# Kernel tuning notes

Measured on AMD Instinct MI355X. Metric: run time of the kernel, lower is better.

Reference implementation:

```python
import jax, jax.numpy as jnp
from jax import lax
import numpy as np

N_DFT = 1024
N_HOP = 256
N_FILTER = N_DFT // 2 + 1  # 513
AMIN = 1e-10
DYNAMIC_RANGE = 80.0


def _make_dft_kernels(n_dft):
    """Real/imag DFT kernels with periodic Hann window, shape (n_dft, 1, n_filter) for WIO conv."""
    nb = n_dft // 2 + 1
    t = np.arange(n_dft)
    w = np.arange(nb) * 2.0 * np.pi / float(n_dft)
    real = np.cos(w[:, None] * t[None, :])           # (nb, n_dft)
    imag = -np.sin(w[:, None] * t[None, :])
    # scipy periodic ('fftbins=True') hann window
    win = 0.5 - 0.5 * np.cos(2.0 * np.pi * t / float(n_dft))
    real = (real * win).T[:, None, :]                # (n_dft, 1, nb) = (W, I, O)
    imag = (imag * win).T[:, None, :]
    return real.astype(np.float32), imag.astype(np.float32)


def setup_inputs() -> dict:
    key = jax.random.key(0)
    x = jax.random.normal(key, (32, 2, 262144), dtype=jnp.float32)  # (batch, n_ch, len_src)
    kr, ki = _make_dft_kernels(N_DFT)
    return {"x": x, "k_real": jnp.asarray(kr), "k_imag": jnp.asarray(ki)}


def reference(x, k_real, k_imag):
    B, CH, L = x.shape
    xm = x.reshape(B * CH, L, 1)  # treat each audio channel as an independent mono signal
    dn = ("NWC", "WIO", "NWC")
    conv = lambda k: lax.conv_general_dilated(
        xm, k, window_strides=(N_HOP,), padding="SAME", dimension_numbers=dn
    )
    # power spectrogram: real^2 + imag^2 -> (B*CH, n_frame, n_filter)
    power = conv(k_real) ** 2 + conv(k_imag) ** 2
    n_frame = power.shape[1]
    # -> (B, n_filter, n_frame, CH)  (channels_last image format)
    spec = power.reshape(B, CH, n_frame, N_FILTER).transpose(0, 3, 2, 1)
    # power_spectrogram == 2.0, so no pow; return_decibel_spectrogram == True:
    log_spec = 10.0 * jnp.log10(jnp.maximum(spec, AMIN))
    log_spec = log_spec - jnp.max(log_spec, axis=(1, 2, 3), keepdims=True)
    return jnp.maximum(log_spec, -DYNAMIC_RANGE)
```

## Files before the change

kernel.cpp:

```cpp
#include <hip/hip_runtime.h>
#include <math.h>

namespace {
constexpr int NDFT   = 1024;
constexpr int NHOP   = 256;
constexpr int NFILT  = 513;
constexpr int LSRC   = 262144;
constexpr int NFRAME = 1024;
constexpr int PAD_L  = 384;
constexpr long PER_B = (long)NFILT * NFRAME * 2;

constexpr int KT2 = 16;
constexpr int CHUNK_US = 8192;
constexpr size_t WSB2_BYTES = (size_t)8 * KT2 * CHUNK_US * 2;
constexpr size_t PLANE_ELEMS_PER_SIG = 1024 * 512;

constexpr int KT1 = 32;
constexpr size_t WS_B_BYTES = (size_t)8 * KT1 * CHUNK_US * 2;
}

using short8 = __attribute__((ext_vector_type(8))) short;
using f32x4  = __attribute__((ext_vector_type(4))) float;

__device__ __forceinline__ unsigned int f2key(float f) {
    unsigned int u = __float_as_uint(f);
    return (u & 0x80000000u) ? ~u : (u | 0x80000000u);
}
__device__ __forceinline__ float key2f(unsigned int k) {
    return (k & 0x80000000u) ? __uint_as_float(k ^ 0x80000000u) : __uint_as_float(~k);
}
__device__ __forceinline__ unsigned short bf16rn(float v) {
    unsigned int u = __float_as_uint(v);
    return (unsigned short)((u + 0x7fffu + ((u >> 16) & 1u)) >> 16);
}

__global__ void zero_ws(unsigned int* __restrict__ w) {
    if (threadIdx.x < 32) w[threadIdx.x] = 0u;
}

__global__ __launch_bounds__(256) void fold_split(
    const float* __restrict__ x,
    unsigned short* __restrict__ sH, unsigned short* __restrict__ sL,
    unsigned short* __restrict__ dH, unsigned short* __restrict__ dL,
    int sig0)
{
    const int floc = blockIdx.x * 4 + (threadIdx.x >> 6);
    const int grp  = threadIdx.x & 63;
    const int sig  = sig0 + (floc >> 10);
    const int fl   = floc & 1023;
    const long sbase = (long)sig * LSRC;
    const int st   = fl * NHOP - PAD_L;
    const int s0   = grp * 8;

    const float xmid = x[sbase + st + 512];

    float fw[8], bw[8];
    if (fl >= 2 && fl <= 1021) {
        const float4 a0 = *reinterpret_cast<const float4*>(x + sbase + st + s0);
        const float4 a1 = *reinterpret_cast<const float4*>(x + sbase + st + s0 + 4);
        fw[0]=a0.x; fw[1]=a0.y; fw[2]=a0.z; fw[3]=a0.w;
        fw[4]=a1.x; fw[5]=a1.y; fw[6]=a1.z; fw[7]=a1.w;
        const long q0 = sbase + st + 1017 - s0;
        const float4 b0 = *reinterpret_cast<const float4*>(x + q0 - 1);
        const float4 b1 = *reinterpret_cast<const float4*>(x + q0 + 3);
        const float  b2 = x[q0 + 7];
        const float va[8] = {b0.y, b0.z, b0.w, b1.x, b1.y, b1.z, b1.w, b2};
        #pragma unroll
        for (int j = 0; j < 8; ++j) bw[j] = va[7 - j];
    } else {
        #pragma unroll
        for (int j = 0; j < 8; ++j) {
            const int s = s0 + j;
            const int p1 = st + s;
            const int p2 = st + 1024 - s;
            fw[j] = ((unsigned)p1 < (unsigned)LSRC) ? x[sbase + p1] : 0.0f;
            bw[j] = ((unsigned)p2 < (unsigned)LSRC) ? x[sbase + p2] : 0.0f;
        }
    }

    union { unsigned short u[8]; uint4 v; } shv, slv, dhv, dlv;
    #pragma unroll
    for (int j = 0; j < 8; ++j) {
        float x1 = fw[j], x2 = bw[j];
        if (j == 0 && s0 == 0) { x1 = xmid; x2 = 0.0f; }
        const float sm = x1 + x2;
        const float df = x1 - x2;
        const unsigned short h1 = bf16rn(sm);
        shv.u[j] = h1;
        slv.u[j] = bf16rn(sm - __uint_as_float((unsigned int)h1 << 16));
        const unsigned short h2 = bf16rn(df);
        dhv.u[j] = h2;
        dlv.u[j] = bf16rn(df - __uint_as_float((unsigned int)h2 << 16));
    }
    const size_t wo = (size_t)floc * 512 + s0;
    *reinterpret_cast<uint4*>(sH + wo) = shv.v;
    *reinterpret_cast<uint4*>(sL + wo) = slv.v;
    *reinterpret_cast<uint4*>(dH + wo) = dhv.v;
    *reinterpret_cast<uint4*>(dL + wo) = dlv.v;
}

__global__ __launch_bounds__(256) void build_B2(const float* __restrict__ kr,
                                                const float* __restrict__ ki,
                                                unsigned short* __restrict__ wsB)
{
    const int nt = blockIdx.x >> 4;
    const int kt = blockIdx.x & 15;
    unsigned short* chunk = wsB + (size_t)blockIdx.x * CHUNK_US;
    const int col = threadIdx.x >> 1;
    const int h   = threadIdx.x & 1;
    const int bin = nt * 64 + (col & 63);
    const float* src = (col < 64) ? kr : ki;
    #pragma unroll
    for (int j = 0; j < 4; ++j) {
        const int sl = h * 4 + j;
        const int c  = sl & 3;
        union { unsigned short u[8]; uint4 v; } pk;
        #pragma unroll
        for (int i = 0; i < 8; ++i) {
            const int s = kt * 32 + c * 8 + i;
            const int t = (s == 0) ? 512 : s;
            const float v = src[t * NFILT + bin];
            const unsigned short hi = bf16rn(v);
            pk.u[i] = h ? bf16rn(v - __uint_as_float((unsigned int)hi << 16)) : hi;
        }
        *reinterpret_cast<uint4*>(&chunk[col * 64 + ((sl ^ (col & 7)) << 3)]) = pk.v;
    }
}

__global__ __launch_bounds__(256, 2) void spec_gemm2(
    const unsigned short* __restrict__ sH, const unsigned short* __restrict__ sL,
    const unsigned short* __restrict__ dH, const unsigned short* __restrict__ dL,
    const unsigned short* __restrict__ wsB,
    float* __restrict__ out, unsigned int* __restrict__ wmax,
    int sig0, int nsig)
{
    __shared__ unsigned short smem[2 * 128 * 64];

    const int tid  = threadIdx.x;
    const int lane = tid & 63, w = tid >> 6;
    const int wm = w >> 1, wn = w & 1;
    const int l15 = lane & 15, l16 = lane >> 4;

    const int phys = blockIdx.x;
    const int xcd  = phys & 7, slot = phys >> 3;
    const int nt   = slot & 7;
    const int mt   = xcd * nsig + (slot >> 3);
    const int sig  = sig0 + (mt >> 3);
    const int f0   = (mt & 7) * 128;
    const unsigned short* bchunks = wsB + (size_t)nt * KT2 * CHUNK_US;

    const unsigned short* __restrict__ pH = wn ? dH : sH;
    const unsigned short* __restrict__ pL = wn ? dL : sL;

    size_t aoff[4];
    #pragma unroll
    for (int mf = 0; mf < 4; ++mf) {
        const int row = wm * 64 + mf * 16 + l15;
        aoff[mf] = (size_t)(mt * 128 + row) * 512 + l16 * 8;
    }

    f32x4 acc[4][4];
    #pragma unroll
    for (int i = 0; i < 4; ++i)
        #pragma unroll
        for (int j = 0; j < 4; ++j)
            #pragma unroll
            for (int r = 0; r < 4; ++r) acc[i][j][r] = 0.0f;

    #define LOAD_B(ktv, nb)                                                    \
        {                                                                      \
            const char* g = (const char*)(bchunks + (size_t)(ktv) * CHUNK_US); \
            char* l = (char*)smem + (nb) * 16384;                              \
            _Pragma("unroll")                                                  \
            for (int i = 0; i < 4; ++i) {                                      \
                const int off = i * 4096 + w * 1024;                           \
                __builtin_amdgcn_global_load_lds(                              \
                    (const __attribute__((address_space(1))) unsigned int*)(g + off + lane * 16), \
                    (__attribute__((address_space(3))) unsigned int*)(l + off), \
                    16, 0, 0);                                                 \
            }                                                                  \
        }

    #define LOAD_A(ktv, AH, AL)                                                \
        {                                                                      \
            _Pragma("unroll")                                                  \
            for (int mf = 0; mf < 4; ++mf) {                                   \
                const size_t o = aoff[mf] + (size_t)(ktv) * 32;                \
                AH[mf] = *reinterpret_cast<const short8*>(pH + o);             \
                AL[mf] = *reinterpret_cast<const short8*>(pL + o);             \
            }                                                                  \
        }

    #define MFMA_STEP(AH, AL, nb)                                              \
        {                                                                      \
            __builtin_amdgcn_s_setprio(1);                                     \
            _Pragma("unroll")                                                  \
            for (int nf = 0; nf < 4; ++nf) {                                   \
                const int col = wn * 64 + nf * 16 + l15;                       \
                const unsigned short* bb = smem + (nb) * 8192 + col * 64;      \
                const short8 bh = *reinterpret_cast<const short8*>(bb + ((l16 ^ (col & 7)) << 3));       \
                const short8 bl = *reinterpret_cast<const short8*>(bb + (((4 + l16) ^ (col & 7)) << 3)); \
                _Pragma("unroll")                                              \
                for (int mf = 0; mf < 4; ++mf) {                               \
                    acc[mf][nf] = __builtin_amdgcn_mfma_f32_16x16x32_bf16(AH[mf], bh, acc[mf][nf], 0, 0, 0); \
                    acc[mf][nf] = __builtin_amdgcn_mfma_f32_16x16x32_bf16(AL[mf], bh, acc[mf][nf], 0, 0, 0); \
                    acc[mf][nf] = __builtin_amdgcn_mfma_f32_16x16x32_bf16(AH[mf], bl, acc[mf][nf], 0, 0, 0); \
                }                                                              \
            }                                                                  \
            __builtin_amdgcn_s_setprio(0);                                     \
        }

    short8 ah0[4], al0[4], ah1[4], al1[4];

    LOAD_A(0, ah0, al0)
    LOAD_B(0, 0)
    __syncthreads();

    #pragma unroll 1
    for (int kt = 0; kt < KT2; kt += 2) {
        LOAD_A(kt + 1, ah1, al1)
        LOAD_B(kt + 1, 1)
        MFMA_STEP(ah0, al0, 0)
        __syncthreads();
        if (kt + 2 < KT2) {
            LOAD_A(kt + 2, ah0, al0)
            LOAD_B(kt + 2, 0)
        }
        MFMA_STEP(ah1, al1, 1)
        __syncthreads();
    }
    #undef LOAD_A
    #undef LOAD_B
    #undef MFMA_STEP

    if (wn == 0) {
        #pragma unroll
        for (int mf = 0; mf < 4; ++mf)
            #pragma unroll
            for (int nf = 0; nf < 4; ++nf) {
                const int binl = nf * 16 + l15;
                #pragma unroll
                for (int r = 0; r < 4; ++r) {
                    const int row = wm * 64 + mf * 16 + l16 * 4 + r;
                    const float v = acc[mf][nf][r];
                    smem[row * 68 + binl] = bf16rn(v * v);
                }
            }
    }
    __syncthreads();
    if (wn == 1) {
        const int batch = sig >> 1, ch = sig & 1;
        float lmax = -3.0e38f;
        #pragma unroll
        for (int mf = 0; mf < 4; ++mf)
            #pragma unroll
            for (int nf = 0; nf < 4; ++nf) {
                const int binl = nf * 16 + l15;
                const int bin  = nt * 64 + binl;
                #pragma unroll
                for (int r = 0; r < 4; ++r) {
                    const int row = wm * 64 + mf * 16 + l16 * 4 + r;
                    const float v = acc[mf][nf][r];
                    const float re2 = __uint_as_float((unsigned int)smem[row * 68 + binl] << 16);
                    const float p = re2 + v * v;
                    const float d = 10.0f * log10f(fmaxf(p, 1e-10f));
                    const int frame = f0 + row;
                    out[((long)(batch * NFILT + bin) * NFRAME + frame) * 2 + ch] = d;
                    lmax = fmaxf(lmax, d);
                }
            }
        #pragma unroll
        for (int off = 32; off > 0; off >>= 1) lmax = fmaxf(lmax, __shfl_xor(lmax, off));
        if (lane == 0) atomicMax(&wmax[batch], f2key(lmax));
    }
}

__global__ __launch_bounds__(256) void build_B(const float* __restrict__ kr,
                                               const float* __restrict__ ki,
                                               unsigned short* __restrict__ wsB)
{
    const int nt = blockIdx.x >> 5;
    const int kt = blockIdx.x & 31;
    unsigned short* chunk = wsB + (size_t)blockIdx.x * CHUNK_US;
    const int col = threadIdx.x >> 1;
    const int h   = threadIdx.x & 1;
    const int bin = nt * 64 + (col >> 1);
    const float* src = (col & 1) ? ki : kr;
    #pragma unroll
    for (int j = 0; j < 4; ++j) {
        const int sl = h * 4 + j;
        const int c  = sl & 3;
        union { unsigned short u[8]; uint4 v; } pk;
        #pragma unroll
        for (int i = 0; i < 8; ++i) {
            const int t = kt * 32 + c * 8 + i;
            const float v = src[t * NFILT + bin];
            const unsigned short hi = bf16rn(v);
            pk.u[i] = h ? bf16rn(v - __uint_as_float((unsigned int)hi << 16)) : hi;
        }
        *reinterpret_cast<uint4*>(&chunk[col * 64 + ((sl ^ (col & 7)) << 3)]) = pk.v;
    }
}

__global__ __launch_bounds__(256, 2) void spec_gemm_mid(
    const float* __restrict__ x, const unsigned short* __restrict__ wsB,
    float* __restrict__ out, unsigned int* __restrict__ wmax)
{
    __shared__ unsigned short Ad[2][128][64];
    __shared__ unsigned short Bd[2][128][64];

    const int tid  = threadIdx.x;
    const int lane = tid & 63, w = tid >> 6;
    const int wm = w >> 1, wn = w & 1;
    const int l15 = lane & 15, l16 = lane >> 4;
    const int mt = blockIdx.x, nt = blockIdx.y;
    const int sig = mt >> 3, f0 = (mt & 7) * 128;
    const long sb = (long)sig * LSRC;

    const int arow = tid >> 1, ac2 = tid & 1;
    const int abase_p = (f0 + arow) * NHOP - PAD_L + ac2 * 16;
    const unsigned short* bchunks = wsB + (size_t)nt * KT1 * CHUNK_US;

    f32x4 acc[4][4];
    #pragma unroll
    for (int i = 0; i < 4; ++i)
        #pragma unroll
        for (int j = 0; j < 4; ++j)
            #pragma unroll
            for (int r = 0; r < 4; ++r) acc[i][j][r] = 0.0f;

    float va[16];

    #define LOAD_A(ktv)                                                        \
        {                                                                      \
            const int p0 = abase_p + (ktv) * 32;                               \
            if (p0 >= 0 && p0 + 16 <= LSRC) {                                  \
                *reinterpret_cast<float4*>(&va[0])  = *reinterpret_cast<const float4*>(x + sb + p0);      \
                *reinterpret_cast<float4*>(&va[4])  = *reinterpret_cast<const float4*>(x + sb + p0 + 4);  \
                *reinterpret_cast<float4*>(&va[8])  = *reinterpret_cast<const float4*>(x + sb + p0 + 8);  \
                *reinterpret_cast<float4*>(&va[12]) = *reinterpret_cast<const float4*>(x + sb + p0 + 12); \
            } else {                                                           \
                _Pragma("unroll")                                              \
                for (int i = 0; i < 16; ++i) {                                 \
                    const int p = p0 + i;                                      \
                    va[i] = (p >= 0 && p < LSRC) ? x[sb + p] : 0.0f;           \
                }                                                              \
            }                                                                  \
        }

    #define LOAD_B(ktv, nb)                                                    \
        {                                                                      \
            const char* g = (const char*)(bchunks + (size_t)(ktv) * CHUNK_US); \
            char* l = (char*)&Bd[nb][0][0];                                    \
            _Pragma("unroll")                                                  \
            for (int i = 0; i < 4; ++i) {                                      \
                const int off = i * 4096 + w * 1024;                           \
                __builtin_amdgcn_global_load_lds(                              \
                    (const __attribute__((address_space(1))) unsigned int*)(g + off + lane * 16), \
                    (__attribute__((address_space(3))) unsigned int*)(l + off), \
                    16, 0, 0);                                                 \
            }                                                                  \
        }

    #define WRITE_A(nb)                                                       \
        {                                                                      \
            unsigned short* ab = &Ad[nb][arow][0];                             \
            _Pragma("unroll")                                                  \
            for (int j = 0; j < 2; ++j) {                                      \
                union { unsigned short u[8]; uint4 v; } hv, lv;                \
                _Pragma("unroll")                                              \
                for (int i = 0; i < 8; ++i) {                                  \
                    const float vv = va[j * 8 + i];                            \
                    const unsigned short hi = bf16rn(vv);                      \
                    hv.u[i] = hi;                                              \
                    lv.u[i] = bf16rn(vv - __uint_as_float((unsigned int)hi << 16)); \
                }                                                              \
                const int c = ac2 * 2 + j;                                     \
                *reinterpret_cast<uint4*>(ab + (((c) ^ (arow & 7)) << 3))     = hv.v; \
                *reinterpret_cast<uint4*>(ab + (((4 + c) ^ (arow & 7)) << 3)) = lv.v; \
            }                                                                  \
        }

    LOAD_A(0)
    LOAD_B(0, 0)
    WRITE_A(0)
    __syncthreads();

    #pragma unroll 1
    for (int kt = 0; kt < KT1; ++kt) {
        const int cur = kt & 1, nxt = cur ^ 1;
        const bool pf = (kt + 1 < KT1);
        if (pf) {
            LOAD_A(kt + 1)
            LOAD_B(kt + 1, nxt)
        }
        short8 ah[4], al[4];
        #pragma unroll
        for (int mf = 0; mf < 4; ++mf) {
            const int row = wm * 64 + mf * 16 + l15;
            const unsigned short* ab = &Ad[cur][row][0];
            ah[mf] = *reinterpret_cast<const short8*>(ab + ((l16 ^ (row & 7)) << 3));
            al[mf] = *reinterpret_cast<const short8*>(ab + (((4 + l16) ^ (row & 7)) << 3));
        }
        __builtin_amdgcn_s_setprio(1);
        #pragma unroll
        for (int nf = 0; nf < 4; ++nf) {
            const int col = wn * 64 + nf * 16 + l15;
            const unsigned short* bb = &Bd[cur][col][0];
            const short8 bh = *reinterpret_cast<const short8*>(bb + ((l16 ^ (col & 7)) << 3));
            const short8 bl = *reinterpret_cast<const short8*>(bb + (((4 + l16) ^ (col & 7)) << 3));
            #pragma unroll
            for (int mf = 0; mf < 4; ++mf) {
                acc[mf][nf] = __builtin_amdgcn_mfma_f32_16x16x32_bf16(ah[mf], bh, acc[mf][nf], 0, 0, 0);
                acc[mf][nf] = __builtin_amdgcn_mfma_f32_16x16x32_bf16(al[mf], bh, acc[mf][nf], 0, 0, 0);
                acc[mf][nf] = __builtin_amdgcn_mfma_f32_16x16x32_bf16(ah[mf], bl, acc[mf][nf], 0, 0, 0);
            }
        }
        __builtin_amdgcn_s_setprio(0);
        if (pf) WRITE_A(nxt)
        __syncthreads();
    }
    #undef LOAD_A
    #undef LOAD_B
    #undef WRITE_A

    const int batch = sig >> 1, ch = sig & 1;
    float lmax = -3.0e38f;
    #pragma unroll
    for (int mf = 0; mf < 4; ++mf)
        #pragma unroll
        for (int nf = 0; nf < 4; ++nf) {
            const int col = nt * 128 + wn * 64 + nf * 16 + l15;
            const int bin = col >> 1;
            #pragma unroll
            for (int r = 0; r < 4; ++r) {
                const float v  = acc[mf][nf][r];
                const float sq = v * v;
                const float p  = sq + __shfl_xor(sq, 1);
                if (!(lane & 1)) {
                    const int frame = f0 + wm * 64 + mf * 16 + l16 * 4 + r;
                    const float d = 10.0f * log10f(fmaxf(p, 1e-10f));
                    out[((long)(batch * NFILT + bin) * NFRAME + frame) * 2 + ch] = d;
                    lmax = fmaxf(lmax, d);
                }
            }
        }
    #pragma unroll
    for (int off = 32; off > 0; off >>= 1) lmax = fmaxf(lmax, __shfl_xor(lmax, off));
    if (lane == 0) atomicMax(&wmax[batch], f2key(lmax));
}

__global__ __launch_bounds__(256, 2) void spec_nyq(
    const float* __restrict__ x, const float* __restrict__ kr,
    const float* __restrict__ ki, float* __restrict__ out,
    unsigned int* __restrict__ wmax)
{
    __shared__ float xs[17152];
    __shared__ float kc[1024], ks[1024];
    const int sig = blockIdx.x >> 4, ft = blockIdx.x & 15;
    const int f0 = ft * 64;
    const long sb = (long)sig * LSRC;
    const int start = f0 * NHOP - PAD_L;
    for (int i = threadIdx.x; i < 17152; i += 256) {
        const int p = start + i;
        xs[i] = (p >= 0 && p < LSRC) ? x[sb + p] : 0.0f;
    }
    for (int t = threadIdx.x; t < 1024; t += 256) {
        kc[t] = kr[t * NFILT + 512];
        ks[t] = ki[t * NFILT + 512];
    }
    __syncthreads();
    const int fr = threadIdx.x >> 2, q = threadIdx.x & 3;
    const int rot = ((fr + q) & 7) * 4;
    float re = 0.0f, im = 0.0f;
    #pragma unroll 4
    for (int j = 0; j < 256; j += 4) {
        const int je = (j + rot) & 255;
        const float4 a = *reinterpret_cast<const float4*>(&xs[fr * 256 + q * 256 + je]);
        const float4 c = *reinterpret_cast<const float4*>(&kc[q * 256 + je]);
        const float4 s = *reinterpret_cast<const float4*>(&ks[q * 256 + je]);
        re = fmaf(a.x, c.x, re); re = fmaf(a.y, c.y, re);
        re = fmaf(a.z, c.z, re); re = fmaf(a.w, c.w, re);
        im = fmaf(a.x, s.x, im); im = fmaf(a.y, s.y, im);
        im = fmaf(a.z, s.z, im); im = fmaf(a.w, s.w, im);
    }
    re += __shfl_xor(re, 1); re += __shfl_xor(re, 2);
    im += __shfl_xor(im, 1); im += __shfl_xor(im, 2);
    const int batch = sig >> 1, ch = sig & 1;
    float lmax = -3.0e38f;
    if (q == 0) {
        const float p = re * re + im * im;
        const float d = 10.0f * log10f(fmaxf(p, 1e-10f));
        out[((long)(batch * NFILT + 512) * NFRAME + (f0 + fr)) * 2 + ch] = d;
        lmax = d;
    }
    #pragma unroll
    for (int off = 32; off > 0; off >>= 1) lmax = fmaxf(lmax, __shfl_xor(lmax, off));
    if ((threadIdx.x & 63) == 0) atomicMax(&wmax[batch], f2key(lmax));
}

__global__ __launch_bounds__(256) void finalize(
    float* __restrict__ out, const unsigned int* __restrict__ wmax, long n4)
{
    const long stride = (long)gridDim.x * 256;
    for (long i4 = blockIdx.x * 256L + threadIdx.x; i4 < n4; i4 += stride) {
        const long i = i4 * 4;
        const int b  = (int)(i / PER_B);
        const float m = key2f(wmax[b]);
        float4 v = reinterpret_cast<float4*>(out)[i4];
        v.x = fmaxf(v.x - m, -80.0f);
        v.y = fmaxf(v.y - m, -80.0f);
        v.z = fmaxf(v.z - m, -80.0f);
        v.w = fmaxf(v.w - m, -80.0f);
        reinterpret_cast<float4*>(out)[i4] = v;
    }
}

namespace fb {
constexpr int TILE_F = 32;
constexpr int SPAN   = (TILE_F - 1) * NHOP + NDFT;
}

__global__ __launch_bounds__(256) void spec_main_fb(
    const float* __restrict__ x, const float* __restrict__ kr,
    const float* __restrict__ ki, float* __restrict__ out,
    unsigned int* __restrict__ wmax)
{
    __shared__ float xs[fb::SPAN];
    const int s   = blockIdx.x;
    const int f0  = blockIdx.y * fb::TILE_F;
    const int tid = threadIdx.x;
    const long sig_base = (long)s * LSRC;
    const int start = f0 * NHOP - PAD_L;
    for (int i = tid; i < fb::SPAN; i += 256) {
        const int p = start + i;
        xs[i] = (p >= 0 && p < LSRC) ? x[sig_base + p] : 0.0f;
    }
    __syncthreads();
    const int b0 = tid, b1 = tid + 256;
    float ar0[fb::TILE_F], ai0[fb::TILE_F], ar1[fb::TILE_F], ai1[fb::TILE_F];
    #pragma unroll
    for (int f = 0; f < fb::TILE_F; ++f) { ar0[f]=0.f; ai0[f]=0.f; ar1[f]=0.f; ai1[f]=0.f; }
    #pragma unroll 1
    for (int t = 0; t < NDFT; t += 4) {
        float br0[4], bq0[4], br1[4], bq1[4];
        #pragma unroll
        for (int j = 0; j < 4; ++j) {
            br0[j] = kr[(t + j) * NFILT + b0]; bq0[j] = ki[(t + j) * NFILT + b0];
            br1[j] = kr[(t + j) * NFILT + b1]; bq1[j] = ki[(t + j) * NFILT + b1];
        }
        #pragma unroll
        for (int f = 0; f < fb::TILE_F; ++f) {
            const float4 a = *reinterpret_cast<const float4*>(&xs[t + NHOP * f]);
            ar0[f]=fmaf(a.x,br0[0],ar0[f]); ar0[f]=fmaf(a.y,br0[1],ar0[f]);
            ar0[f]=fmaf(a.z,br0[2],ar0[f]); ar0[f]=fmaf(a.w,br0[3],ar0[f]);
            ai0[f]=fmaf(a.x,bq0[0],ai0[f]); ai0[f]=fmaf(a.y,bq0[1],ai0[f]);
            ai0[f]=fmaf(a.z,bq0[2],ai0[f]); ai0[f]=fmaf(a.w,bq0[3],ai0[f]);
            ar1[f]=fmaf(a.x,br1[0],ar1[f]); ar1[f]=fmaf(a.y,br1[1],ar1[f]);
            ar1[f]=fmaf(a.z,br1[2],ar1[f]); ar1[f]=fmaf(a.w,br1[3],ar1[f]);
            ai1[f]=fmaf(a.x,bq1[0],ai1[f]); ai1[f]=fmaf(a.y,bq1[1],ai1[f]);
            ai1[f]=fmaf(a.z,bq1[2],ai1[f]); ai1[f]=fmaf(a.w,bq1[3],ai1[f]);
        }
    }
    const int b = s >> 1, ch = s & 1;
    float lmax = -3.0e38f;
    #pragma unroll
    for (int f = 0; f < fb::TILE_F; ++f) {
        const int frame = f0 + f;
        const float p0 = ar0[f]*ar0[f] + ai0[f]*ai0[f];
        const float p1 = ar1[f]*ar1[f] + ai1[f]*ai1[f];
        const float d0 = 10.0f * log10f(fmaxf(p0, 1e-10f));
        const float d1 = 10.0f * log10f(fmaxf(p1, 1e-10f));
        lmax = fmaxf(lmax, fmaxf(d0, d1));
        out[((long)(b * NFILT + b0) * NFRAME + frame) * 2 + ch] = d0;
        out[((long)(b * NFILT + b1) * NFRAME + frame) * 2 + ch] = d1;
    }
    #pragma unroll
    for (int off = 32; off > 0; off >>= 1) lmax = fmaxf(lmax, __shfl_xor(lmax, off));
    if ((tid & 63) == 0) atomicMax(&wmax[b], f2key(lmax));
}

__global__ __launch_bounds__(256) void spec_nyq_fb(
    const float* __restrict__ x, const float* __restrict__ kr,
    const float* __restrict__ ki, float* __restrict__ out,
    unsigned int* __restrict__ wmax)
{
    const int gid   = blockIdx.x * 256 + threadIdx.x;
    const int s     = gid >> 10;
    const int frame = gid & 1023;
    const float* xp = x + (long)s * LSRC;
    const int start = frame * NHOP - PAD_L;
    float re = 0.f, im = 0.f;
    for (int t = 0; t < NDFT; ++t) {
        const int idx = start + t;
        const float a = (idx >= 0 && idx < LSRC) ? xp[idx] : 0.0f;
        re = fmaf(a, kr[t * NFILT + 512], re);
        im = fmaf(a, ki[t * NFILT + 512], im);
    }
    const float p = re * re + im * im;
    const float d = 10.0f * log10f(fmaxf(p, 1e-10f));
    const int b = s >> 1, ch = s & 1;
    out[((long)(b * NFILT + 512) * NFRAME + frame) * 2 + ch] = d;
    float lmax = d;
    #pragma unroll
    for (int off = 32; off > 0; off >>= 1) lmax = fmaxf(lmax, __shfl_xor(lmax, off));
    if ((threadIdx.x & 63) == 0) atomicMax(&wmax[b], f2key(lmax));
}

extern "C" void kernel_launch(void* const* d_in, const int* in_sizes, int n_in,
                              void* d_out, int out_size, void* d_ws, size_t ws_size,
                              hipStream_t stream) {
    const float* x  = (const float*)d_in[0];
    const float* kr = (const float*)d_in[1];
    const float* ki = (const float*)d_in[2];
    float* out = (float*)d_out;
    const long n4 = (long)out_size / 4;

    int nsig = 0;
    const int cands[4] = {64, 32, 16, 8};
    for (int c = 0; c < 4; ++c) {
        const size_t need = 128 + WSB2_BYTES + (size_t)cands[c] * 4 * 1048576;
        if (ws_size >= need) { nsig = cands[c]; break; }
    }

    if (nsig) {
        unsigned int* wmax   = (unsigned int*)d_ws;
        unsigned short* wsB2 = (unsigned short*)((char*)d_ws + 128);
        unsigned short* sH   = (unsigned short*)((char*)d_ws + 128 + WSB2_BYTES);
        const size_t pe = (size_t)nsig * PLANE_ELEMS_PER_SIG;
        unsigned short* sL = sH + pe;
        unsigned short* dH = sL + pe;
        unsigned short* dL = dH + pe;
        zero_ws<<<1, 64, 0, stream>>>(wmax);
        build_B2<<<128, 256, 0, stream>>>(kr, ki, wsB2);
        const int npass = 64 / nsig;
        for (int p = 0; p < npass; ++p) {
            fold_split<<<nsig * 256, 256, 0, stream>>>(x, sH, sL, dH, dL, p * nsig);
            spec_gemm2<<<nsig * 64, 256, 0, stream>>>(sH, sL, dH, dL, wsB2, out, wmax,
                                                      p * nsig, nsig);
        }
        spec_nyq<<<1024, 256, 0, stream>>>(x, kr, ki, out, wmax);
        finalize<<<2048, 256, 0, stream>>>(out, wmax, n4);
    } else if (ws_size >= WS_B_BYTES + 128) {
        unsigned short* wsB = (unsigned short*)d_ws;
        unsigned int* wmax  = (unsigned int*)((char*)d_ws + WS_B_BYTES);
        zero_ws<<<1, 64, 0, stream>>>(wmax);
        build_B<<<8 * KT1, 256, 0, stream>>>(kr, ki, wsB);
        spec_gemm_mid<<<dim3(512, 8), 256, 0, stream>>>(x, wsB, out, wmax);
        spec_nyq<<<1024, 256, 0, stream>>>(x, kr, ki, out, wmax);
        finalize<<<2048, 256, 0, stream>>>(out, wmax, n4);
    } else {
        unsigned int* wmax = (unsigned int*)d_ws;
        zero_ws<<<1, 64, 0, stream>>>(wmax);
        dim3 grid(64, NFRAME / fb::TILE_F);
        spec_main_fb<<<grid, 256, 0, stream>>>(x, kr, ki, out, wmax);
        spec_nyq_fb<<<(64 * NFRAME) / 256, 256, 0, stream>>>(x, kr, ki, out, wmax);
        finalize<<<2048, 256, 0, stream>>>(out, wmax, n4);
    }
}
```

Before: 622.7 us.

## Split spec_gemm2 across 8 waves with narrower per-wave tiles and single A buffer

Doubles the block to 512 threads (8 waves), so each wave computes a 64x32 output tile instead of 64x64. A-fragment register double buffering is removed: A for the next k-step is now loaded after the current MFMA step, which cuts register use and allows more resident waves (launch bounds 512,4). The B LDS load is split across more waves. The cost is less latency hiding for A loads, since each load is issued just before the barrier, and more redundant A loads per block because wave pairs share rows.

```diff
diff --git a/kernel.cpp b/kernel.cpp
--- a/kernel.cpp
+++ b/kernel.cpp
@@ -127,7 +127,7 @@
     }
 }
 
-__global__ __launch_bounds__(256, 2) void spec_gemm2(
+__global__ __launch_bounds__(512, 4) void spec_gemm2(
     const unsigned short* __restrict__ sH, const unsigned short* __restrict__ sL,
     const unsigned short* __restrict__ dH, const unsigned short* __restrict__ dL,
     const unsigned short* __restrict__ wsB,
@@ -138,7 +138,7 @@
 
     const int tid  = threadIdx.x;
     const int lane = tid & 63, w = tid >> 6;
-    const int wm = w >> 1, wn = w & 1;
+    const int wm = w >> 2, wn = w & 3;
     const int l15 = lane & 15, l16 = lane >> 4;
 
     const int phys = blockIdx.x;
@@ -149,21 +149,16 @@
     const int f0   = (mt & 7) * 128;
     const unsigned short* bchunks = wsB + (size_t)nt * KT2 * CHUNK_US;
 
-    const unsigned short* __restrict__ pH = wn ? dH : sH;
-    const unsigned short* __restrict__ pL = wn ? dL : sL;
-
-    size_t aoff[4];
-    #pragma unroll
-    for (int mf = 0; mf < 4; ++mf) {
-        const int row = wm * 64 + mf * 16 + l15;
-        aoff[mf] = (size_t)(mt * 128 + row) * 512 + l16 * 8;
-    }
-
-    f32x4 acc[4][4];
+    const unsigned short* __restrict__ pH = (wn >= 2) ? dH : sH;
+    const unsigned short* __restrict__ pL = (wn >= 2) ? dL : sL;
+
+    const size_t abase = (size_t)(mt * 128 + wm * 64 + l15) * 512 + l16 * 8;
+
+    f32x4 acc[4][2];
     #pragma unroll
     for (int i = 0; i < 4; ++i)
         #pragma unroll
-        for (int j = 0; j < 4; ++j)
+        for (int j = 0; j < 2; ++j)
             #pragma unroll
             for (int r = 0; r < 4; ++r) acc[i][j][r] = 0.0f;
 
@@ -172,8 +167,8 @@
             const char* g = (const char*)(bchunks + (size_t)(ktv) * CHUNK_US); \
             char* l = (char*)smem + (nb) * 16384;                              \
             _Pragma("unroll")                                                  \
-            for (int i = 0; i < 4; ++i) {                                      \
-                const int off = i * 4096 + w * 1024;                           \
+            for (int i = 0; i < 2; ++i) {                                      \
+                const int off = i * 8192 + w * 1024;                           \
                 __builtin_amdgcn_global_load_lds(                              \
                     (const __attribute__((address_space(1))) unsigned int*)(g + off + lane * 16), \
                     (__attribute__((address_space(3))) unsigned int*)(l + off), \
@@ -181,64 +176,62 @@
             }                                                                  \
         }
 
-    #define LOAD_A(ktv, AH, AL)                                                \
+    #define LOAD_A(ktv)                                                        \
         {                                                                      \
             _Pragma("unroll")                                                  \
             for (int mf = 0; mf < 4; ++mf) {                                   \
-                const size_t o = aoff[mf] + (size_t)(ktv) * 32;                \
-                AH[mf] = *reinterpret_cast<const short8*>(pH + o);             \
-                AL[mf] = *reinterpret_cast<const short8*>(pL + o);             \
+                const size_t o = abase + (size_t)mf * 8192 + (size_t)(ktv) * 32; \
+                ah[mf] = *reinterpret_cast<const short8*>(pH + o);             \
+                al[mf] = *reinterpret_cast<const short8*>(pL + o);             \
             }                                                                  \
         }
 
-    #define MFMA_STEP(AH, AL, nb)                                              \
+    #define MFMA_STEP(nb)                                                      \
         {                                                                      \
             __builtin_amdgcn_s_setprio(1);                                     \
             _Pragma("unroll")                                                  \
-            for (int nf = 0; nf < 4; ++nf) {                                   \
-                const int col = wn * 64 + nf * 16 + l15;                       \
+            for (int nf = 0; nf < 2; ++nf) {                                   \
+                const int col = wn * 32 + nf * 16 + l15;                       \
                 const unsigned short* bb = smem + (nb) * 8192 + col * 64;      \
                 const short8 bh = *reinterpret_cast<const short8*>(bb + ((l16 ^ (col & 7)) << 3));       \
                 const short8 bl = *reinterpret_cast<const short8*>(bb + (((4 + l16) ^ (col & 7)) << 3)); \
                 _Pragma("unroll")                                              \
                 for (int mf = 0; mf < 4; ++mf) {                               \
-                    acc[mf][nf] = __builtin_amdgcn_mfma_f32_16x16x32_bf16(AH[mf], bh, acc[mf][nf], 0, 0, 0); \
-                    acc[mf][nf] = __builtin_amdgcn_mfma_f32_16x16x32_bf16(AL[mf], bh, acc[mf][nf], 0, 0, 0); \
-                    acc[mf][nf] = __builtin_amdgcn_mfma_f32_16x16x32_bf16(AH[mf], bl, acc[mf][nf], 0, 0, 0); \
+                    acc[mf][nf] = __builtin_amdgcn_mfma_f32_16x16x32_bf16(ah[mf], bh, acc[mf][nf], 0, 0, 0); \
+                    acc[mf][nf] = __builtin_amdgcn_mfma_f32_16x16x32_bf16(al[mf], bh, acc[mf][nf], 0, 0, 0); \
+                    acc[mf][nf] = __builtin_amdgcn_mfma_f32_16x16x32_bf16(ah[mf], bl, acc[mf][nf], 0, 0, 0); \
                 }                                                              \
             }                                                                  \
             __builtin_amdgcn_s_setprio(0);                                     \
         }
 
-    short8 ah0[4], al0[4], ah1[4], al1[4];
-
-    LOAD_A(0, ah0, al0)
+    short8 ah[4], al[4];
+
+    LOAD_A(0)
     LOAD_B(0, 0)
     __syncthreads();
 
     #pragma unroll 1
     for (int kt = 0; kt < KT2; kt += 2) {
-        LOAD_A(kt + 1, ah1, al1)
         LOAD_B(kt + 1, 1)
-        MFMA_STEP(ah0, al0, 0)
+        MFMA_STEP(0)
+        LOAD_A(kt + 1)
         __syncthreads();
-        if (kt + 2 < KT2) {
-            LOAD_A(kt + 2, ah0, al0)
-            LOAD_B(kt + 2, 0)
-        }
-        MFMA_STEP(ah1, al1, 1)
+        if (kt + 2 < KT2) LOAD_B(kt + 2, 0)
+        MFMA_STEP(1)
+        if (kt + 2 < KT2) LOAD_A(kt + 2)
         __syncthreads();
     }
     #undef LOAD_A
     #undef LOAD_B
     #undef MFMA_STEP
 
-    if (wn == 0) {
+    if (wn < 2) {
         #pragma unroll
         for (int mf = 0; mf < 4; ++mf)
             #pragma unroll
-            for (int nf = 0; nf < 4; ++nf) {
-                const int binl = nf * 16 + l15;
+            for (int nf = 0; nf < 2; ++nf) {
+                const int binl = wn * 32 + nf * 16 + l15;
                 #pragma unroll
                 for (int r = 0; r < 4; ++r) {
                     const int row = wm * 64 + mf * 16 + l16 * 4 + r;
@@ -248,14 +241,14 @@
             }
     }
     __syncthreads();
-    if (wn == 1) {
+    if (wn >= 2) {
         const int batch = sig >> 1, ch = sig & 1;
         float lmax = -3.0e38f;
         #pragma unroll
         for (int mf = 0; mf < 4; ++mf)
             #pragma unroll
-            for (int nf = 0; nf < 4; ++nf) {
-                const int binl = nf * 16 + l15;
+            for (int nf = 0; nf < 2; ++nf) {
+                const int binl = (wn - 2) * 32 + nf * 16 + l15;
                 const int bin  = nt * 64 + binl;
                 #pragma unroll
                 for (int r = 0; r < 4; ++r) {
@@ -636,7 +629,7 @@
         const int npass = 64 / nsig;
         for (int p = 0; p < npass; ++p) {
             fold_split<<<nsig * 256, 256, 0, stream>>>(x, sH, sL, dH, dL, p * nsig);
-            spec_gemm2<<<nsig * 64, 256, 0, stream>>>(sH, sL, dH, dL, wsB2, out, wmax,
+            spec_gemm2<<<nsig * 64, 512, 0, stream>>>(sH, sL, dH, dL, wsB2, out, wmax,
                                                       p * nsig, nsig);
         }
         spec_nyq<<<1024, 256, 0, stream>>>(x, kr, ki, out, wmax);
```

Result: slower. 812.2 us (+30.4%).

## Load B fragments directly from global into registers, dropping LDS staging and barriers

Applied to the files above, without the earlier changes.

The GEMM kernel previously staged B chunks into double-buffered shared memory via global_load_lds and synchronized with barriers each k-step. It now loads each wave's B fragments straight from global memory into registers, double-buffered alongside A, and removes the per-step __syncthreads. This cuts LDS traffic, shared memory footprint and barrier stalls, but adds duplicated global/L2 reads of B across waves and more register pressure under launch_bounds(256,2). Shared memory is shrunk to 128x68 for the epilogue use only.

```diff
diff --git a/kernel.cpp b/kernel.cpp
--- a/kernel.cpp
+++ b/kernel.cpp
@@ -134,7 +134,7 @@
     float* __restrict__ out, unsigned int* __restrict__ wmax,
     int sig0, int nsig)
 {
-    __shared__ unsigned short smem[2 * 128 * 64];
+    __shared__ unsigned short smem[128 * 68];
 
     const int tid  = threadIdx.x;
     const int lane = tid & 63, w = tid >> 6;
@@ -158,6 +158,13 @@
         const int row = wm * 64 + mf * 16 + l15;
         aoff[mf] = (size_t)(mt * 128 + row) * 512 + l16 * 8;
     }
+    int boff_h[4], boff_l[4];
+    #pragma unroll
+    for (int nf = 0; nf < 4; ++nf) {
+        const int col = wn * 64 + nf * 16 + l15;
+        boff_h[nf] = col * 64 + ((l16 ^ (col & 7)) << 3);
+        boff_l[nf] = col * 64 + (((4 + l16) ^ (col & 7)) << 3);
+    }
 
     f32x4 acc[4][4];
     #pragma unroll
@@ -166,20 +173,6 @@
         for (int j = 0; j < 4; ++j)
             #pragma unroll
             for (int r = 0; r < 4; ++r) acc[i][j][r] = 0.0f;
-
-    #define LOAD_B(ktv, nb)                                                    \
-        {                                                                      \
-            const char* g = (const char*)(bchunks + (size_t)(ktv) * CHUNK_US); \
-            char* l = (char*)smem + (nb) * 16384;                              \
-            _Pragma("unroll")                                                  \
-            for (int i = 0; i < 4; ++i) {                                      \
-                const int off = i * 4096 + w * 1024;                           \
-                __builtin_amdgcn_global_load_lds(                              \
-                    (const __attribute__((address_space(1))) unsigned int*)(g + off + lane * 16), \
-                    (__attribute__((address_space(3))) unsigned int*)(l + off), \
-                    16, 0, 0);                                                 \
-            }                                                                  \
-        }
 
     #define LOAD_A(ktv, AH, AL)                                                \
         {                                                                      \
@@ -191,43 +184,51 @@
             }                                                                  \
         }
 
-    #define MFMA_STEP(AH, AL, nb)                                              \
+    #define LOAD_B(ktv, BH, BL)                                                \
+        {                                                                      \
+            const unsigned short* c = bchunks + (size_t)(ktv) * CHUNK_US;      \
+            _Pragma("unroll")                                                  \
+            for (int nf = 0; nf < 4; ++nf) {                                   \
+                BH[nf] = *reinterpret_cast<const short8*>(c + boff_h[nf]);     \
+                BL[nf] = *reinterpret_cast<const short8*>(c + boff_l[nf]);     \
+            }                                                                  \
+        }
+
+    #define MFMA_STEP(AH, AL, BH, BL)                                          \
         {                                                                      \
             __builtin_amdgcn_s_setprio(1);                                     \
             _Pragma("unroll")                                                  \
             for (int nf = 0; nf < 4; ++nf) {                                   \
-                const int col = wn * 64 + nf * 16 + l15;                       \
-                const unsigned short* bb = smem + (nb) * 8192 + col * 64;      \
-                const short8 bh = *reinterpret_cast<const short8*>(bb + ((l16 ^ (col & 7)) << 3));       \
-                const short8 bl = *reinterpret_cast<const short8*>(bb + (((4 + l16) ^ (col & 7)) << 3)); \
                 _Pragma("unroll")                                              \
                 for (int mf = 0; mf < 4; ++mf) {                               \
-                    acc[mf][nf] = __builtin_amdgcn_mfma_f32_16x16x32_bf16(AH[mf], bh, acc[mf][nf], 0, 0, 0); \
-                    acc[mf][nf] = __builtin_amdgcn_mfma_f32_16x16x32_bf16(AL[mf], bh, acc[mf][nf], 0, 0, 0); \
-                    acc[mf][nf] = __builtin_amdgcn_mfma_f32_16x16x32_bf16(AH[mf], bl, acc[mf][nf], 0, 0, 0); \
+                    acc[mf][nf] = __builtin_amdgcn_mfma_f32_16x16x32_bf16(AH[mf], BH[nf], acc[mf][nf], 0, 0, 0); \
+                    acc[mf][nf] = __builtin_amdgcn_mfma_f32_16x16x32_bf16(AL[mf], BH[nf], acc[mf][nf], 0, 0, 0); \
+                    acc[mf][nf] = __builtin_amdgcn_mfma_f32_16x16x32_bf16(AH[mf], BL[nf], acc[mf][nf], 0, 0, 0); \
                 }                                                              \
             }                                                                  \
             __builtin_amdgcn_s_setprio(0);                                     \
         }
 
     short8 ah0[4], al0[4], ah1[4], al1[4];
+    short8 bh0[4], bl0[4], bh1[4], bl1[4];
 
     LOAD_A(0, ah0, al0)
-    LOAD_B(0, 0)
-    __syncthreads();
+    LOAD_B(0, bh0, bl0)
+    LOAD_A(1, ah1, al1)
+    LOAD_B(1, bh1, bl1)
 
     #pragma unroll 1
     for (int kt = 0; kt < KT2; kt += 2) {
-        LOAD_A(kt + 1, ah1, al1)
-        LOAD_B(kt + 1, 1)
-        MFMA_STEP(ah0, al0, 0)
-        __syncthreads();
+        MFMA_STEP(ah0, al0, bh0, bl0)
         if (kt + 2 < KT2) {
             LOAD_A(kt + 2, ah0, al0)
-            LOAD_B(kt + 2, 0)
-        }
-        MFMA_STEP(ah1, al1, 1)
-        __syncthreads();
+            LOAD_B(kt + 2, bh0, bl0)
+        }
+        MFMA_STEP(ah1, al1, bh1, bl1)
+        if (kt + 3 < KT2) {
+            LOAD_A(kt + 3, ah1, al1)
+            LOAD_B(kt + 3, bh1, bl1)
+        }
     }
     #undef LOAD_A
     #undef LOAD_B
```

Measured after the change: 626.5 us. No clear change (+0.6%).

## Stage A tiles through LDS via direct global-to-LDS loads in spec_gemm2

Applied to the files above, without the earlier changes.

The A operand (hi/lo bf16 frames) is now loaded from global memory straight into LDS with swizzled global_load_lds, rather than being read into registers per wave. The B tile follows the same path, and the wave layout is remapped so each wn pair shares its own A/B region. The software double buffering is dropped in favour of a simple stage, sync, compute, sync loop, which lowers register pressure and may coalesce A reads better. In exchange, loads no longer overlap with MFMA work inside a block and each k-step adds barriers.

```diff
diff --git a/kernel.cpp b/kernel.cpp
--- a/kernel.cpp
+++ b/kernel.cpp
@@ -134,11 +134,11 @@
     float* __restrict__ out, unsigned int* __restrict__ wmax,
     int sig0, int nsig)
 {
-    __shared__ unsigned short smem[2 * 128 * 64];
+    __shared__ unsigned short smem[24576];
 
     const int tid  = threadIdx.x;
     const int lane = tid & 63, w = tid >> 6;
-    const int wm = w >> 1, wn = w & 1;
+    const int wm = w & 1, wn = w >> 1;
     const int l15 = lane & 15, l16 = lane >> 4;
 
     const int phys = blockIdx.x;
@@ -152,12 +152,18 @@
     const unsigned short* __restrict__ pH = wn ? dH : sH;
     const unsigned short* __restrict__ pL = wn ? dL : sL;
 
-    size_t aoff[4];
-    #pragma unroll
-    for (int mf = 0; mf < 4; ++mf) {
-        const int row = wm * 64 + mf * 16 + l15;
-        aoff[mf] = (size_t)(mt * 128 + row) * 512 + l16 * 8;
-    }
+    const int rl = lane >> 3, jj = lane & 7;
+    const int q  = jj ^ rl;
+    const unsigned short* apl = (q < 4) ? pH : pL;
+    const unsigned short* agsrc[8];
+    #pragma unroll
+    for (int i = 0; i < 8; ++i)
+        agsrc[i] = apl + (size_t)(mt * 128 + wm * 64 + i * 8 + rl) * 512 + (q & 3) * 8;
+
+    unsigned short* Areg  = smem + wn * 12288;
+    unsigned short* Breg  = Areg + 8192;
+    unsigned short* aldst = Areg + wm * 4096;
+    unsigned short* bldst = Breg + wm * 2048;
 
     f32x4 acc[4][4];
     #pragma unroll
@@ -167,71 +173,61 @@
             #pragma unroll
             for (int r = 0; r < 4; ++r) acc[i][j][r] = 0.0f;
 
-    #define LOAD_B(ktv, nb)                                                    \
-        {                                                                      \
-            const char* g = (const char*)(bchunks + (size_t)(ktv) * CHUNK_US); \
-            char* l = (char*)smem + (nb) * 16384;                              \
-            _Pragma("unroll")                                                  \
-            for (int i = 0; i < 4; ++i) {                                      \
-                const int off = i * 4096 + w * 1024;                           \
-                __builtin_amdgcn_global_load_lds(                              \
-                    (const __attribute__((address_space(1))) unsigned int*)(g + off + lane * 16), \
-                    (__attribute__((address_space(3))) unsigned int*)(l + off), \
-                    16, 0, 0);                                                 \
-            }                                                                  \
-        }
-
-    #define LOAD_A(ktv, AH, AL)                                                \
+    #define STAGE(ktv)                                                         \
         {                                                                      \
             _Pragma("unroll")                                                  \
+            for (int i = 0; i < 8; ++i)                                        \
+                __builtin_amdgcn_global_load_lds(                              \
+                    (const __attribute__((address_space(1))) unsigned int*)(agsrc[i] + (ktv) * 32), \
+                    (__attribute__((address_space(3))) unsigned int*)(aldst + i * 512), \
+                    16, 0, 0);                                                 \
+            const unsigned short* gBs = bchunks + (size_t)(ktv) * CHUNK_US + wn * 4096 + wm * 2048; \
+            _Pragma("unroll")                                                  \
+            for (int i = 0; i < 4; ++i)                                        \
+                __builtin_amdgcn_global_load_lds(                              \
+                    (const __attribute__((address_space(1))) unsigned int*)(gBs + i * 512 + lane * 8), \
+                    (__attribute__((address_space(3))) unsigned int*)(bldst + i * 512), \
+                    16, 0, 0);                                                 \
+        }
+
+    #define COMPUTE()                                                          \
+        {                                                                      \
+            short8 ah[4], al[4], bh[4], bl[4];                                 \
+            _Pragma("unroll")                                                  \
             for (int mf = 0; mf < 4; ++mf) {                                   \
-                const size_t o = aoff[mf] + (size_t)(ktv) * 32;                \
-                AH[mf] = *reinterpret_cast<const short8*>(pH + o);             \
-                AL[mf] = *reinterpret_cast<const short8*>(pL + o);             \
+                const int row = wm * 64 + mf * 16 + l15;                       \
+                const unsigned short* ab = Areg + row * 64;                    \
+                ah[mf] = *reinterpret_cast<const short8*>(ab + ((l16 ^ (row & 7)) << 3));        \
+                al[mf] = *reinterpret_cast<const short8*>(ab + (((4 + l16) ^ (row & 7)) << 3));  \
             }                                                                  \
-        }
-
-    #define MFMA_STEP(AH, AL, nb)                                              \
-        {                                                                      \
+            _Pragma("unroll")                                                  \
+            for (int nf = 0; nf < 4; ++nf) {                                   \
+                const int coll = nf * 16 + l15;                                \
+                const unsigned short* bb = Breg + coll * 64;                   \
+                bh[nf] = *reinterpret_cast<const short8*>(bb + ((l16 ^ (coll & 7)) << 3));       \
+                bl[nf] = *reinterpret_cast<const short8*>(bb + (((4 + l16) ^ (coll & 7)) << 3)); \
+            }                                                                  \
             __builtin_amdgcn_s_setprio(1);                                     \
             _Pragma("unroll")                                                  \
-            for (int nf = 0; nf < 4; ++nf) {                                   \
-                const int col = wn * 64 + nf * 16 + l15;                       \
-                const unsigned short* bb = smem + (nb) * 8192 + col * 64;      \
-                const short8 bh = *reinterpret_cast<const short8*>(bb + ((l16 ^ (col & 7)) << 3));       \
-                const short8 bl = *reinterpret_cast<const short8*>(bb + (((4 + l16) ^ (col & 7)) << 3)); \
+            for (int nf = 0; nf < 4; ++nf)                                     \
                 _Pragma("unroll")                                              \
                 for (int mf = 0; mf < 4; ++mf) {                               \
-                    acc[mf][nf] = __builtin_amdgcn_mfma_f32_16x16x32_bf16(AH[mf], bh, acc[mf][nf], 0, 0, 0); \
-                    acc[mf][nf] = __builtin_amdgcn_mfma_f32_16x16x32_bf16(AL[mf], bh, acc[mf][nf], 0, 0, 0); \
-                    acc[mf][nf] = __builtin_amdgcn_mfma_f32_16x16x32_bf16(AH[mf], bl, acc[mf][nf], 0, 0, 0); \
+                    acc[mf][nf] = __builtin_amdgcn_mfma_f32_16x16x32_bf16(ah[mf], bh[nf], acc[mf][nf], 0, 0, 0); \
+                    acc[mf][nf] = __builtin_amdgcn_mfma_f32_16x16x32_bf16(al[mf], bh[nf], acc[mf][nf], 0, 0, 0); \
+                    acc[mf][nf] = __builtin_amdgcn_mfma_f32_16x16x32_bf16(ah[mf], bl[nf], acc[mf][nf], 0, 0, 0); \
                 }                                                              \
-            }                                                                  \
             __builtin_amdgcn_s_setprio(0);                                     \
         }
 
-    short8 ah0[4], al0[4], ah1[4], al1[4];
-
-    LOAD_A(0, ah0, al0)
-    LOAD_B(0, 0)
-    __syncthreads();
-
     #pragma unroll 1
-    for (int kt = 0; kt < KT2; kt += 2) {
-        LOAD_A(kt + 1, ah1, al1)
-        LOAD_B(kt + 1, 1)
-        MFMA_STEP(ah0, al0, 0)
+    for (int kt = 0; kt < KT2; ++kt) {
+        STAGE(kt)
         __syncthreads();
-        if (kt + 2 < KT2) {
-            LOAD_A(kt + 2, ah0, al0)
-            LOAD_B(kt + 2, 0)
-        }
-        MFMA_STEP(ah1, al1, 1)
+        COMPUTE()
         __syncthreads();
     }
-    #undef LOAD_A
-    #undef LOAD_B
-    #undef MFMA_STEP
+    #undef STAGE
+    #undef COMPUTE
 
     if (wn == 0) {
         #pragma unroll
```

After: 540.3 us. 1.15x faster.
